# Performance work log

Measured on AMD Instinct MI355X. Metric: run time of the kernel, lower is better.

Reference implementation:

```python
import jax, jax.numpy as jnp
import numpy as np

B = 4096      # batch
F = 16        # num fields
V = 20000     # field vocab size
E = 64        # embed size
HID = 1024    # hidden width (all hidden layers equal, required by the reshape trick)
NODE_IN = F * E  # 1024
NL = 3        # number of hidden layers stacked into attention (len(layer_sizes)-2)


def _xavier(key, shape):
    fan_in, fan_out = shape[0], shape[1]
    lim = np.sqrt(6.0 / (fan_in + fan_out)).astype(np.float32)
    return jax.random.uniform(key, shape, jnp.float32, -lim, lim)


def setup_inputs() -> dict:
    key = jax.random.key(0)
    ks = jax.random.split(key, 8)
    idx = jax.random.randint(ks[0], (B, F), 0, V)
    emb = _xavier(ks[1], (V, E))  # share init shape, then tile per-field via fold_in
    emb = jnp.stack([_xavier(jax.random.fold_in(ks[1], f), (V, E)) for f in range(F)], axis=0)  # [F,V,E]
    w0 = _xavier(ks[2], (NODE_IN, HID)); b0 = jnp.zeros((HID,), jnp.float32)
    w1 = _xavier(ks[3], (HID, HID));     b1 = jnp.zeros((HID,), jnp.float32)
    w2 = _xavier(ks[4], (HID, HID));     b2 = jnp.zeros((HID,), jnp.float32)
    w3 = _xavier(ks[5], (HID, HID));     b3 = jnp.zeros((HID,), jnp.float32)
    w_final = _xavier(ks[6], (2 * HID, 1)); b_final = jnp.zeros((1,), jnp.float32)
    return {"idx": idx, "emb": emb, "w0": w0, "b0": b0, "w1": w1, "b1": b1,
            "w2": w2, "b2": b2, "w3": w3, "b3": b3,
            "w_final": w_final, "b_final": b_final}


def reference(idx, emb, w0, b0, w1, b1, w2, b2, w3, b3, w_final, b_final):
    bsz = idx.shape[0]
    # sparse one-hot @ embed == gather: [B,F,E] -> [B, F*E]
    xw = emb[jnp.arange(F)[None, :], idx].reshape(bsz, F * E)
    # MLP stack (dropout in test mode: keep_prob=1, i.e. identity)
    l0 = jax.nn.relu(xw @ w0 + b0)
    l1 = jax.nn.relu(l0 @ w1 + b1)
    l2 = jax.nn.relu(l1 @ w2 + b2)
    l_final = jax.nn.relu(l2 @ w3 + b3)
    # faithful reproduction of tf.concat(axis=0) then reshape([-1, NL, HID])
    cat = jnp.concatenate([l0, l1, l2], axis=0)          # [NL*B, HID]
    Hm = cat.reshape(bsz, NL, HID)                        # H[b,j] = cat[NL*b + j]
    mask = 1.0 - jnp.eye(NL, dtype=Hm.dtype)              # zero diagonal
    S = jnp.einsum('bih,bjh->bij', Hm, Hm) * mask         # [B, NL, NL]
    A = jax.nn.softmax(S, axis=-1)                        # attention over layers
    G = jnp.einsum('bij,bjh->bh', A, Hm)                  # reduce_sum(A@H, axis=1)
    M = jnp.concatenate([l_final, G], axis=1)             # [B, 2*HID]
    out = (M @ w_final + b_final).squeeze(-1)             # logits [B]
    return out
```

## Files before the change

kernel.cpp:

```cpp
#include <hip/hip_runtime.h>
#include <hip/hip_bf16.h>
#include <stdint.h>

#define B_SZ 4096
#define F_N 16
#define V_SZ 20000
#define E_SZ 64
#define HID 1024

typedef __attribute__((ext_vector_type(8))) _Float16 f16x8;
typedef __attribute__((ext_vector_type(4))) _Float16 f16x4;
typedef __attribute__((ext_vector_type(4))) float f32x4;

__device__ __forceinline__ void gload16(const void* g, void* l) {
  __builtin_amdgcn_global_load_lds(
      (const __attribute__((address_space(1))) void*)g,
      (__attribute__((address_space(3))) void*)l, 16, 0, 0);
}

__device__ __forceinline__ int s3(int r) { return (r ^ (r >> 3)) & 7; }

__global__ __launch_bounds__(256) void prep(
    const int* __restrict__ idx, const float* __restrict__ emb,
    const float* __restrict__ w0, const float* __restrict__ w1,
    const float* __restrict__ w2, const float* __restrict__ w3,
    _Float16* __restrict__ wt, _Float16* __restrict__ xw) {
  const int cb = blockIdx.x;
  const int t = threadIdx.x;
  if (cb < 2048) {
    const int z = cb >> 9, rem = cb & 511;
    const float* w = (z == 0) ? w0 : (z == 1) ? w1 : (z == 2) ? w2 : w3;
    _Float16* outp = wt + (size_t)z * HID * HID;
    __shared__ float tile[64][33];
    const int k0 = (rem >> 5) * 64, n0 = (rem & 31) * 32;
    const int c = t & 31;
#pragma unroll
    for (int q = 0; q < 8; ++q) {
      int r = (t >> 5) + q * 8;
      tile[r][c] = w[(size_t)(k0 + r) * HID + n0 + c];
    }
    __syncthreads();
#pragma unroll
    for (int q = 0; q < 4; ++q) {
      int s = t + q * 256;
      int n = s >> 5, c2 = s & 31;
      _Float16 lo = (_Float16)tile[2 * c2][n];
      _Float16 hi = (_Float16)tile[2 * c2 + 1][n];
      union { _Float16 h[2]; uint32_t u; } p;
      p.h[0] = lo; p.h[1] = hi;
      *(uint32_t*)(outp + (size_t)(n0 + n) * HID + k0 + 2 * c2) = p.u;
    }
  } else {
    int i = (cb - 2048) * 256 + t;
    int b = i >> 8;
    int r = i & 255;
    int f = r >> 4;
    int e4 = r & 15;
    int id = idx[b * F_N + f];
    float4 v = *(const float4*)(emb + ((size_t)f * V_SZ + id) * E_SZ + e4 * 4);
    f16x4 h = {(_Float16)v.x, (_Float16)v.y, (_Float16)v.z, (_Float16)v.w};
    *(f16x4*)(xw + (size_t)b * HID + r * 4) = h;
  }
}

__global__ __launch_bounds__(512) void gemm_mfma(
    const _Float16* __restrict__ A, const _Float16* __restrict__ Wt,
    const float* __restrict__ bias, _Float16* __restrict__ C) {
  __shared__ __align__(16) _Float16 sh[2][2][128 * 64];
#define AS(b) (sh[b][0])
#define BS(b) (sh[b][1])

  const int t = threadIdx.x;
  const int l = ((blockIdx.x & 7) << 5) | (blockIdx.x >> 3);
  const int bm = (l >> 3) * 128, bn = (l & 7) * 128;

  const int w = t >> 6, lane = t & 63;
  const int wk = w & 1, wn = (w >> 1) & 1, wm = w >> 2;
  const int lr = lane & 15, lg = lane >> 4;

  const int srow = t >> 3, cdst = t & 7;
  const int csrc = cdst ^ s3(srow);
  const _Float16* ga0 = A + (size_t)(bm + srow) * HID + csrc * 8;
  const _Float16* gb0 = Wt + (size_t)(bn + srow) * HID + csrc * 8;
  const int ld0 = t * 8, ld1 = t * 8 + 4096;

  int aoff[4], boff[4];
#pragma unroll
  for (int i = 0; i < 4; i++) {
    int ra = wm * 64 + i * 16 + lr;
    aoff[i] = ra * 64 + (((wk * 4 + lg) ^ s3(ra)) * 8);
    int rb = wn * 64 + i * 16 + lr;
    boff[i] = rb * 64 + (((wk * 4 + lg) ^ s3(rb)) * 8);
  }

  f32x4 acc[4][4] = {};

#define STAGE(buf, ko)                                   \
  gload16(ga0 + (ko), &AS(buf)[ld0]);                    \
  gload16(ga0 + (ko) + (size_t)64 * HID, &AS(buf)[ld1]); \
  gload16(gb0 + (ko), &BS(buf)[ld0]);                    \
  gload16(gb0 + (ko) + (size_t)64 * HID, &BS(buf)[ld1]);

  STAGE(0, 0)

  for (int tI = 0; tI < 16; ++tI) {
    const int cur = tI & 1;
    if (tI < 15) {
      STAGE(cur ^ 1, (tI + 1) * 64)
    }
    if (tI < 15)
      asm volatile("s_waitcnt vmcnt(4)" ::: "memory");
    else
      asm volatile("s_waitcnt vmcnt(0)" ::: "memory");
    asm volatile("s_barrier" ::: "memory");

    f16x8 a[4], b[4];
#pragma unroll
    for (int mi = 0; mi < 4; mi++) a[mi] = *(const f16x8*)&AS(cur)[aoff[mi]];
#pragma unroll
    for (int ni = 0; ni < 4; ni++) b[ni] = *(const f16x8*)&BS(cur)[boff[ni]];
#pragma unroll
    for (int mi = 0; mi < 4; mi++)
#pragma unroll
      for (int ni = 0; ni < 4; ni++)
        acc[mi][ni] = __builtin_amdgcn_mfma_f32_16x16x32_f16(
            a[mi], b[ni], acc[mi][ni], 0, 0, 0);

    asm volatile("s_barrier" ::: "memory");
  }
#undef STAGE

  float* red = (float*)&sh[0][0][0];
  float* R = red + ((wm << 1) | wn) * 4096;
  if (wk == 1) {
#pragma unroll
    for (int mi = 0; mi < 4; mi++)
#pragma unroll
      for (int ni = 0; ni < 4; ni++) {
        int col = ni * 16 + lr;
        int rb = mi * 4 + lg;
        *(f32x4*)&R[col * 64 + ((rb ^ (col & 15)) << 2)] = acc[mi][ni];
      }
  }
  asm volatile("s_barrier" ::: "memory");
  if (wk == 0) {
#pragma unroll
    for (int mi = 0; mi < 4; mi++)
#pragma unroll
      for (int ni = 0; ni < 4; ni++) {
        int col = ni * 16 + lr;
        int rb = mi * 4 + lg;
        f32x4 p = *(const f32x4*)&R[col * 64 + ((rb ^ (col & 15)) << 2)];
        acc[mi][ni] += p;
      }
#pragma unroll
    for (int ni = 0; ni < 4; ni++) {
      int col = bn + wn * 64 + ni * 16 + lr;
      float bv = bias[col];
#pragma unroll
      for (int mi = 0; mi < 4; mi++) {
        int rbase = bm + wm * 64 + mi * 16 + lg * 4;
#pragma unroll
        for (int j = 0; j < 4; j++) {
          float x = acc[mi][ni][j] + bv;
          x = x > 0.f ? x : 0.f;
          C[(size_t)(rbase + j) * HID + col] = (_Float16)x;
        }
      }
    }
  }
#undef AS
#undef BS
}

__global__ __launch_bounds__(256) void attn_final(
    const _Float16* __restrict__ cat, const _Float16* __restrict__ lf,
    const float* __restrict__ wf, const float* __restrict__ bfin,
    float* __restrict__ out) {
  const int wave = threadIdx.x >> 6;
  const int lane = threadIdx.x & 63;
  const int b = blockIdx.x * 4 + wave;

  const _Float16* h0 = cat + (size_t)(3 * b + 0) * 1024;
  const _Float16* h1 = cat + (size_t)(3 * b + 1) * 1024;
  const _Float16* h2 = cat + (size_t)(3 * b + 2) * 1024;
  const _Float16* lfr = lf + (size_t)b * 1024;

  float s01 = 0.f, s02 = 0.f, s12 = 0.f;
  float d0 = 0.f, d1 = 0.f, d2 = 0.f, dl = 0.f;

#pragma unroll
  for (int q = 0; q < 2; ++q) {
    int e8 = (lane + q * 64) * 8;
    f16x8 a0 = *(const f16x8*)(h0 + e8);
    f16x8 a1 = *(const f16x8*)(h1 + e8);
    f16x8 a2 = *(const f16x8*)(h2 + e8);
    f16x8 al = *(const f16x8*)(lfr + e8);
    float4 u0a = *(const float4*)(wf + e8);
    float4 u0b = *(const float4*)(wf + e8 + 4);
    float4 u1a = *(const float4*)(wf + 1024 + e8);
    float4 u1b = *(const float4*)(wf + 1024 + e8 + 4);
    float wf0[8] = {u0a.x, u0a.y, u0a.z, u0a.w, u0b.x, u0b.y, u0b.z, u0b.w};
    float wf1[8] = {u1a.x, u1a.y, u1a.z, u1a.w, u1b.x, u1b.y, u1b.z, u1b.w};
#pragma unroll
    for (int j = 0; j < 8; ++j) {
      float p0 = (float)a0[j], p1 = (float)a1[j], p2 = (float)a2[j];
      float pl = (float)al[j];
      s01 = fmaf(p0, p1, s01);
      s02 = fmaf(p0, p2, s02);
      s12 = fmaf(p1, p2, s12);
      d0 = fmaf(p0, wf1[j], d0);
      d1 = fmaf(p1, wf1[j], d1);
      d2 = fmaf(p2, wf1[j], d2);
      dl = fmaf(pl, wf0[j], dl);
    }
  }

#pragma unroll
  for (int m = 1; m < 64; m <<= 1) {
    s01 += __shfl_xor(s01, m);
    s02 += __shfl_xor(s02, m);
    s12 += __shfl_xor(s12, m);
    d0 += __shfl_xor(d0, m);
    d1 += __shfl_xor(d1, m);
    d2 += __shfl_xor(d2, m);
    dl += __shfl_xor(dl, m);
  }

  if (lane == 0) {
    float c0 = 0.f, c1 = 0.f, c2 = 0.f;
    {
      float m = fmaxf(0.f, fmaxf(s01, s02));
      float e0 = expf(0.f - m), e1 = expf(s01 - m), e2 = expf(s02 - m);
      float inv = 1.f / (e0 + e1 + e2);
      c0 += e0 * inv; c1 += e1 * inv; c2 += e2 * inv;
    }
    {
      float m = fmaxf(s01, fmaxf(0.f, s12));
      float e0 = expf(s01 - m), e1 = expf(0.f - m), e2 = expf(s12 - m);
      float inv = 1.f / (e0 + e1 + e2);
      c0 += e0 * inv; c1 += e1 * inv; c2 += e2 * inv;
    }
    {
      float m = fmaxf(s02, fmaxf(s12, 0.f));
      float e0 = expf(s02 - m), e1 = expf(s12 - m), e2 = expf(0.f - m);
      float inv = 1.f / (e0 + e1 + e2);
      c0 += e0 * inv; c1 += e1 * inv; c2 += e2 * inv;
    }
    out[b] = dl + c0 * d0 + c1 * d1 + c2 * d2 + bfin[0];
  }
}

extern "C" void kernel_launch(void* const* d_in, const int* in_sizes, int n_in,
                              void* d_out, int out_size, void* d_ws,
                              size_t ws_size, hipStream_t stream) {
  const int* idx = (const int*)d_in[0];
  const float* emb = (const float*)d_in[1];
  const float* w0 = (const float*)d_in[2];
  const float* b0 = (const float*)d_in[3];
  const float* w1 = (const float*)d_in[4];
  const float* b1 = (const float*)d_in[5];
  const float* w2 = (const float*)d_in[6];
  const float* b2 = (const float*)d_in[7];
  const float* w3 = (const float*)d_in[8];
  const float* b3 = (const float*)d_in[9];
  const float* wf = (const float*)d_in[10];
  const float* bfin = (const float*)d_in[11];
  float* out = (float*)d_out;

  const size_t RB = (size_t)B_SZ * HID;
  const size_t WSZ = (size_t)HID * HID;

  _Float16* wt = (_Float16*)d_ws;
  _Float16* xw16 = wt + 4 * WSZ;
  _Float16* cat16 = xw16 + RB;
  _Float16* lf16 = cat16 + 3 * RB;

  prep<<<6144, 256, 0, stream>>>(idx, emb, w0, w1, w2, w3, wt, xw16);

  gemm_mfma<<<256, 512, 0, stream>>>(xw16, wt + 0 * WSZ, b0, cat16);
  gemm_mfma<<<256, 512, 0, stream>>>(cat16, wt + 1 * WSZ, b1, cat16 + RB);
  gemm_mfma<<<256, 512, 0, stream>>>(cat16 + RB, wt + 2 * WSZ, b2,
                                     cat16 + 2 * RB);
  gemm_mfma<<<256, 512, 0, stream>>>(cat16 + 2 * RB, wt + 3 * WSZ, b3, lf16);

  attn_final<<<B_SZ / 4, 256, 0, stream>>>(cat16, lf16, wf, bfin, out);
}
```

Measured before the change: 73.23 us.

## Overlap weight conversion with previous GEMM and load B directly to registers

Converting and transposing the next layer's weights now happens in extra blocks (256..511) of the preceding GEMM launch, so the prep kernel only handles w0 and the embedding gather. The GEMM now reads B fragments straight from global memory into registers instead of staging them through LDS. A becomes a triple-buffered LDS pipeline with explicit waitcnt, sched barriers and setprio around the MFMAs. This is meant to hide prep cost and cut LDS traffic and barriers, at the cost of uncoalesced global B loads and heavier register use.

```diff
diff --git a/kernel.cpp b/kernel.cpp
--- a/kernel.cpp
+++ b/kernel.cpp
@@ -22,36 +22,31 @@
 
 __global__ __launch_bounds__(256) void prep(
     const int* __restrict__ idx, const float* __restrict__ emb,
-    const float* __restrict__ w0, const float* __restrict__ w1,
-    const float* __restrict__ w2, const float* __restrict__ w3,
-    _Float16* __restrict__ wt, _Float16* __restrict__ xw) {
+    const float* __restrict__ w0, _Float16* __restrict__ wt0,
+    _Float16* __restrict__ xw) {
   const int cb = blockIdx.x;
   const int t = threadIdx.x;
-  if (cb < 2048) {
-    const int z = cb >> 9, rem = cb & 511;
-    const float* w = (z == 0) ? w0 : (z == 1) ? w1 : (z == 2) ? w2 : w3;
-    _Float16* outp = wt + (size_t)z * HID * HID;
+  if (cb < 512) {
     __shared__ float tile[64][33];
-    const int k0 = (rem >> 5) * 64, n0 = (rem & 31) * 32;
+    const int k0 = (cb >> 5) * 64, n0 = (cb & 31) * 32;
     const int c = t & 31;
 #pragma unroll
     for (int q = 0; q < 8; ++q) {
       int r = (t >> 5) + q * 8;
-      tile[r][c] = w[(size_t)(k0 + r) * HID + n0 + c];
+      tile[r][c] = w0[(size_t)(k0 + r) * HID + n0 + c];
     }
     __syncthreads();
 #pragma unroll
     for (int q = 0; q < 4; ++q) {
       int s = t + q * 256;
       int n = s >> 5, c2 = s & 31;
-      _Float16 lo = (_Float16)tile[2 * c2][n];
-      _Float16 hi = (_Float16)tile[2 * c2 + 1][n];
       union { _Float16 h[2]; uint32_t u; } p;
-      p.h[0] = lo; p.h[1] = hi;
-      *(uint32_t*)(outp + (size_t)(n0 + n) * HID + k0 + 2 * c2) = p.u;
+      p.h[0] = (_Float16)tile[2 * c2][n];
+      p.h[1] = (_Float16)tile[2 * c2 + 1][n];
+      *(uint32_t*)(wt0 + (size_t)(n0 + n) * HID + k0 + 2 * c2) = p.u;
     }
   } else {
-    int i = (cb - 2048) * 256 + t;
+    int i = (cb - 512) * 256 + t;
     int b = i >> 8;
     int r = i & 255;
     int f = r >> 4;
@@ -65,12 +60,34 @@
 
 __global__ __launch_bounds__(512) void gemm_mfma(
     const _Float16* __restrict__ A, const _Float16* __restrict__ Wt,
-    const float* __restrict__ bias, _Float16* __restrict__ C) {
-  __shared__ __align__(16) _Float16 sh[2][2][128 * 64];
-#define AS(b) (sh[b][0])
-#define BS(b) (sh[b][1])
-
+    const float* __restrict__ bias, _Float16* __restrict__ C,
+    const float* __restrict__ wnx, _Float16* __restrict__ wtnx) {
+  __shared__ __align__(16) char shraw[65536];
   const int t = threadIdx.x;
+
+  if (blockIdx.x >= 256) {
+    const int cv = blockIdx.x - 256;
+    float (*tile)[65] = (float(*)[65])shraw;
+    const int k0 = (cv >> 4) * 64, n0 = (cv & 15) * 64;
+    const int c = t & 63;
+#pragma unroll
+    for (int q = 0; q < 8; ++q) {
+      int r = (t >> 6) + q * 8;
+      tile[r][c] = wnx[(size_t)(k0 + r) * HID + n0 + c];
+    }
+    __syncthreads();
+    {
+      int n = t >> 3, ch = t & 7;
+      f16x8 v;
+#pragma unroll
+      for (int j = 0; j < 8; ++j) v[j] = (_Float16)tile[ch * 8 + j][n];
+      *(f16x8*)(wtnx + (size_t)(n0 + n) * HID + k0 + ch * 8) = v;
+    }
+    return;
+  }
+
+#define AS(b) ((_Float16*)(shraw + (b) * 16384))
+
   const int l = ((blockIdx.x & 7) << 5) | (blockIdx.x >> 3);
   const int bm = (l >> 3) * 128, bn = (l & 7) * 128;
 
@@ -81,56 +98,83 @@
   const int srow = t >> 3, cdst = t & 7;
   const int csrc = cdst ^ s3(srow);
   const _Float16* ga0 = A + (size_t)(bm + srow) * HID + csrc * 8;
-  const _Float16* gb0 = Wt + (size_t)(bn + srow) * HID + csrc * 8;
   const int ld0 = t * 8, ld1 = t * 8 + 4096;
 
-  int aoff[4], boff[4];
+  int aoff[4];
 #pragma unroll
   for (int i = 0; i < 4; i++) {
     int ra = wm * 64 + i * 16 + lr;
     aoff[i] = ra * 64 + (((wk * 4 + lg) ^ s3(ra)) * 8);
-    int rb = wn * 64 + i * 16 + lr;
-    boff[i] = rb * 64 + (((wk * 4 + lg) ^ s3(rb)) * 8);
-  }
+  }
+
+  const _Float16* gB[4];
+#pragma unroll
+  for (int ni = 0; ni < 4; ni++)
+    gB[ni] = Wt + (size_t)(bn + wn * 64 + ni * 16 + lr) * HID + wk * 32 + lg * 8;
 
   f32x4 acc[4][4] = {};
+  f16x8 bE[4], bO[4];
 
 #define STAGE(buf, ko)                                   \
   gload16(ga0 + (ko), &AS(buf)[ld0]);                    \
-  gload16(ga0 + (ko) + (size_t)64 * HID, &AS(buf)[ld1]); \
-  gload16(gb0 + (ko), &BS(buf)[ld0]);                    \
-  gload16(gb0 + (ko) + (size_t)64 * HID, &BS(buf)[ld1]);
+  gload16(ga0 + (ko) + (size_t)64 * HID, &AS(buf)[ld1]);
+
+#define LOADB(dst, ko)                                             \
+  _Pragma("unroll") for (int ni = 0; ni < 4; ni++)                 \
+      dst[ni] = *(const f16x8*)(gB[ni] + (ko));
+
+#define COMPUTE(BUF, BREG)                                                   \
+  {                                                                          \
+    f16x8 a[4];                                                              \
+    _Pragma("unroll") for (int mi = 0; mi < 4; mi++)                         \
+        a[mi] = *(const f16x8*)&AS(BUF)[aoff[mi]];                           \
+    __builtin_amdgcn_s_setprio(1);                                           \
+    _Pragma("unroll") for (int mi = 0; mi < 4; mi++)                         \
+        _Pragma("unroll") for (int ni = 0; ni < 4; ni++)                     \
+            acc[mi][ni] = __builtin_amdgcn_mfma_f32_16x16x32_f16(            \
+                a[mi], BREG[ni], acc[mi][ni], 0, 0, 0);                      \
+    __builtin_amdgcn_s_setprio(0);                                           \
+  }
 
   STAGE(0, 0)
-
-  for (int tI = 0; tI < 16; ++tI) {
-    const int cur = tI & 1;
-    if (tI < 15) {
-      STAGE(cur ^ 1, (tI + 1) * 64)
-    }
-    if (tI < 15)
-      asm volatile("s_waitcnt vmcnt(4)" ::: "memory");
+  __builtin_amdgcn_sched_barrier(0);
+  LOADB(bE, 0)
+  __builtin_amdgcn_sched_barrier(0);
+  STAGE(1, 64)
+
+#pragma unroll
+  for (int u = 0; u < 8; ++u) {
+    const int ta = 2 * u, tb = 2 * u + 1;
+    asm volatile("s_waitcnt vmcnt(2)" ::: "memory");
+    asm volatile("s_barrier" ::: "memory");
+    LOADB(bO, (ta + 1) * 64)
+    __builtin_amdgcn_sched_barrier(0);
+    if (ta + 2 < 16) {
+      STAGE((ta + 2) % 3, (ta + 2) * 64)
+    }
+    __builtin_amdgcn_sched_barrier(0);
+    COMPUTE(ta % 3, bE)
+    if (tb == 15)
+      asm volatile("s_waitcnt vmcnt(0)" ::: "memory");
     else
-      asm volatile("s_waitcnt vmcnt(0)" ::: "memory");
+      asm volatile("s_waitcnt vmcnt(2)" ::: "memory");
     asm volatile("s_barrier" ::: "memory");
-
-    f16x8 a[4], b[4];
-#pragma unroll
-    for (int mi = 0; mi < 4; mi++) a[mi] = *(const f16x8*)&AS(cur)[aoff[mi]];
-#pragma unroll
-    for (int ni = 0; ni < 4; ni++) b[ni] = *(const f16x8*)&BS(cur)[boff[ni]];
-#pragma unroll
-    for (int mi = 0; mi < 4; mi++)
-#pragma unroll
-      for (int ni = 0; ni < 4; ni++)
-        acc[mi][ni] = __builtin_amdgcn_mfma_f32_16x16x32_f16(
-            a[mi], b[ni], acc[mi][ni], 0, 0, 0);
-
-    asm volatile("s_barrier" ::: "memory");
-  }
+    if (tb + 1 < 16) {
+      LOADB(bE, (tb + 1) * 64)
+    }
+    __builtin_amdgcn_sched_barrier(0);
+    if (tb + 2 < 16) {
+      STAGE((tb + 2) % 3, (tb + 2) * 64)
+    }
+    __builtin_amdgcn_sched_barrier(0);
+    COMPUTE(tb % 3, bO)
+  }
+#undef COMPUTE
+#undef LOADB
 #undef STAGE
 
-  float* red = (float*)&sh[0][0][0];
+  asm volatile("s_barrier" ::: "memory");
+  float* red = (float*)shraw;
   float* R = red + ((wm << 1) | wn) * 4096;
   if (wk == 1) {
 #pragma unroll
@@ -170,7 +214,6 @@
     }
   }
 #undef AS
-#undef BS
 }
 
 __global__ __launch_bounds__(256) void attn_final(
@@ -276,13 +319,17 @@
   _Float16* cat16 = xw16 + RB;
   _Float16* lf16 = cat16 + 3 * RB;
 
-  prep<<<6144, 256, 0, stream>>>(idx, emb, w0, w1, w2, w3, wt, xw16);
-
-  gemm_mfma<<<256, 512, 0, stream>>>(xw16, wt + 0 * WSZ, b0, cat16);
-  gemm_mfma<<<256, 512, 0, stream>>>(cat16, wt + 1 * WSZ, b1, cat16 + RB);
-  gemm_mfma<<<256, 512, 0, stream>>>(cat16 + RB, wt + 2 * WSZ, b2,
-                                     cat16 + 2 * RB);
-  gemm_mfma<<<256, 512, 0, stream>>>(cat16 + 2 * RB, wt + 3 * WSZ, b3, lf16);
+  prep<<<4608, 256, 0, stream>>>(idx, emb, w0, wt, xw16);
+
+  gemm_mfma<<<512, 512, 0, stream>>>(xw16, wt + 0 * WSZ, b0, cat16,
+                                     w1, wt + 1 * WSZ);
+  gemm_mfma<<<512, 512, 0, stream>>>(cat16, wt + 1 * WSZ, b1, cat16 + RB,
+                                     w2, wt + 2 * WSZ);
+  gemm_mfma<<<512, 512, 0, stream>>>(cat16 + RB, wt + 2 * WSZ, b2,
+                                     cat16 + 2 * RB, w3, wt + 3 * WSZ);
+  gemm_mfma<<<256, 512, 0, stream>>>(cat16 + 2 * RB, wt + 3 * WSZ, b3, lf16,
+                                     (const float*)nullptr,
+                                     (_Float16*)nullptr);
 
   attn_final<<<B_SZ / 4, 256, 0, stream>>>(cat16, lf16, wf, bfin, out);
 }
```

After: 124.3 us. 1.7x slower.

## Deepen GEMM K-loop to four LDS stages with register double-buffered fragments

Applied to the files above, without the earlier changes.

The MFMA GEMM main loop moves from a double-buffered LDS ring to a four-slot ring with two tiles in flight, and is unrolled by two. Register fragments are now double-buffered, so the LDS reads for the next tile are issued before the MFMAs for the current tile, with s_setprio raised around the MFMA block. This aims to hide global-load and LDS latency and to drop the second barrier per iteration. In exchange it uses 128KB of LDS per block and more registers, which could limit occupancy.

```diff
diff --git a/kernel.cpp b/kernel.cpp
--- a/kernel.cpp
+++ b/kernel.cpp
@@ -44,10 +44,9 @@
     for (int q = 0; q < 4; ++q) {
       int s = t + q * 256;
       int n = s >> 5, c2 = s & 31;
-      _Float16 lo = (_Float16)tile[2 * c2][n];
-      _Float16 hi = (_Float16)tile[2 * c2 + 1][n];
       union { _Float16 h[2]; uint32_t u; } p;
-      p.h[0] = lo; p.h[1] = hi;
+      p.h[0] = (_Float16)tile[2 * c2][n];
+      p.h[1] = (_Float16)tile[2 * c2 + 1][n];
       *(uint32_t*)(outp + (size_t)(n0 + n) * HID + k0 + 2 * c2) = p.u;
     }
   } else {
@@ -66,9 +65,9 @@
 __global__ __launch_bounds__(512) void gemm_mfma(
     const _Float16* __restrict__ A, const _Float16* __restrict__ Wt,
     const float* __restrict__ bias, _Float16* __restrict__ C) {
-  __shared__ __align__(16) _Float16 sh[2][2][128 * 64];
-#define AS(b) (sh[b][0])
-#define BS(b) (sh[b][1])
+  __shared__ __align__(16) char shraw[131072];
+#define AS(b) ((_Float16*)(shraw + (b) * 32768))
+#define BS(b) ((_Float16*)(shraw + (b) * 32768 + 16384))
 
   const int t = threadIdx.x;
   const int l = ((blockIdx.x & 7) << 5) | (blockIdx.x >> 3);
@@ -94,6 +93,7 @@
   }
 
   f32x4 acc[4][4] = {};
+  f16x8 aE[4], bE[4], aO[4], bO[4];
 
 #define STAGE(buf, ko)                                   \
   gload16(ga0 + (ko), &AS(buf)[ld0]);                    \
@@ -101,36 +101,60 @@
   gload16(gb0 + (ko), &BS(buf)[ld0]);                    \
   gload16(gb0 + (ko) + (size_t)64 * HID, &BS(buf)[ld1]);
 
+#define LOADFRAG(AF, BF, buf)                                      \
+  _Pragma("unroll") for (int i = 0; i < 4; i++) {                  \
+    AF[i] = *(const f16x8*)&AS(buf)[aoff[i]];                      \
+    BF[i] = *(const f16x8*)&BS(buf)[boff[i]];                      \
+  }
+
+#define COMPUTE(AF, BF)                                                      \
+  {                                                                          \
+    __builtin_amdgcn_s_setprio(1);                                          \
+    _Pragma("unroll") for (int mi = 0; mi < 4; mi++)                         \
+        _Pragma("unroll") for (int ni = 0; ni < 4; ni++)                     \
+            acc[mi][ni] = __builtin_amdgcn_mfma_f32_16x16x32_f16(            \
+                AF[mi], BF[ni], acc[mi][ni], 0, 0, 0);                       \
+    __builtin_amdgcn_s_setprio(0);                                          \
+  }
+
   STAGE(0, 0)
-
-  for (int tI = 0; tI < 16; ++tI) {
-    const int cur = tI & 1;
-    if (tI < 15) {
-      STAGE(cur ^ 1, (tI + 1) * 64)
-    }
-    if (tI < 15)
+  STAGE(1, 64)
+  asm volatile("s_waitcnt vmcnt(4)" ::: "memory");
+  asm volatile("s_barrier" ::: "memory");
+  LOADFRAG(aE, bE, 0)
+
+#pragma unroll
+  for (int u = 0; u < 8; ++u) {
+    const int ta = 2 * u, tb = 2 * u + 1;
+    if (ta + 2 < 16) {
+      STAGE((ta + 2) & 3, (ta + 2) * 64)
+    }
+    if (ta < 14)
       asm volatile("s_waitcnt vmcnt(4)" ::: "memory");
-    else
+    else if (ta == 14)
       asm volatile("s_waitcnt vmcnt(0)" ::: "memory");
     asm volatile("s_barrier" ::: "memory");
-
-    f16x8 a[4], b[4];
-#pragma unroll
-    for (int mi = 0; mi < 4; mi++) a[mi] = *(const f16x8*)&AS(cur)[aoff[mi]];
-#pragma unroll
-    for (int ni = 0; ni < 4; ni++) b[ni] = *(const f16x8*)&BS(cur)[boff[ni]];
-#pragma unroll
-    for (int mi = 0; mi < 4; mi++)
-#pragma unroll
-      for (int ni = 0; ni < 4; ni++)
-        acc[mi][ni] = __builtin_amdgcn_mfma_f32_16x16x32_f16(
-            a[mi], b[ni], acc[mi][ni], 0, 0, 0);
-
+    LOADFRAG(aO, bO, (ta + 1) & 3)
+    COMPUTE(aE, bE)
+    if (tb + 2 < 16) {
+      STAGE((tb + 2) & 3, (tb + 2) * 64)
+    }
+    if (tb < 14)
+      asm volatile("s_waitcnt vmcnt(4)" ::: "memory");
+    else if (tb == 14)
+      asm volatile("s_waitcnt vmcnt(0)" ::: "memory");
     asm volatile("s_barrier" ::: "memory");
-  }
+    if (tb < 15) {
+      LOADFRAG(aE, bE, (tb + 1) & 3)
+    }
+    COMPUTE(aO, bO)
+  }
+#undef COMPUTE
+#undef LOADFRAG
 #undef STAGE
 
-  float* red = (float*)&sh[0][0][0];
+  asm volatile("s_barrier" ::: "memory");
+  float* red = (float*)shraw;
   float* R = red + ((wm << 1) | wn) * 4096;
   if (wk == 1) {
 #pragma unroll
```

Result: no change. 74.11 us (+1.2%).

## Overlap next-layer weight transpose with GEMM and vectorize epilogue stores

Applied to the files above, without the earlier changes.

The prep kernel now converts and transposes only w0. Each GEMM launch gets 256 extra blocks that transpose and convert the next layer's weights into fp16, so that work shares the launch with the current GEMM instead of running serially beforehand. The MFMA operand order is swapped so each lane holds four consecutive columns, which allows a float4 bias load and 8-byte f16x4 output stores instead of scalar 2-byte stores. The extra blocks compete with GEMM blocks for CUs and shared memory, and the reduction layout is changed to match the transposed accumulator.

```diff
diff --git a/kernel.cpp b/kernel.cpp
--- a/kernel.cpp
+++ b/kernel.cpp
@@ -22,36 +22,31 @@
 
 __global__ __launch_bounds__(256) void prep(
     const int* __restrict__ idx, const float* __restrict__ emb,
-    const float* __restrict__ w0, const float* __restrict__ w1,
-    const float* __restrict__ w2, const float* __restrict__ w3,
-    _Float16* __restrict__ wt, _Float16* __restrict__ xw) {
+    const float* __restrict__ w0, _Float16* __restrict__ wt0,
+    _Float16* __restrict__ xw) {
   const int cb = blockIdx.x;
   const int t = threadIdx.x;
-  if (cb < 2048) {
-    const int z = cb >> 9, rem = cb & 511;
-    const float* w = (z == 0) ? w0 : (z == 1) ? w1 : (z == 2) ? w2 : w3;
-    _Float16* outp = wt + (size_t)z * HID * HID;
+  if (cb < 512) {
     __shared__ float tile[64][33];
-    const int k0 = (rem >> 5) * 64, n0 = (rem & 31) * 32;
+    const int k0 = (cb >> 5) * 64, n0 = (cb & 31) * 32;
     const int c = t & 31;
 #pragma unroll
     for (int q = 0; q < 8; ++q) {
       int r = (t >> 5) + q * 8;
-      tile[r][c] = w[(size_t)(k0 + r) * HID + n0 + c];
+      tile[r][c] = w0[(size_t)(k0 + r) * HID + n0 + c];
     }
     __syncthreads();
 #pragma unroll
     for (int q = 0; q < 4; ++q) {
       int s = t + q * 256;
       int n = s >> 5, c2 = s & 31;
-      _Float16 lo = (_Float16)tile[2 * c2][n];
-      _Float16 hi = (_Float16)tile[2 * c2 + 1][n];
       union { _Float16 h[2]; uint32_t u; } p;
-      p.h[0] = lo; p.h[1] = hi;
-      *(uint32_t*)(outp + (size_t)(n0 + n) * HID + k0 + 2 * c2) = p.u;
+      p.h[0] = (_Float16)tile[2 * c2][n];
+      p.h[1] = (_Float16)tile[2 * c2 + 1][n];
+      *(uint32_t*)(wt0 + (size_t)(n0 + n) * HID + k0 + 2 * c2) = p.u;
     }
   } else {
-    int i = (cb - 2048) * 256 + t;
+    int i = (cb - 512) * 256 + t;
     int b = i >> 8;
     int r = i & 255;
     int f = r >> 4;
@@ -65,12 +60,35 @@
 
 __global__ __launch_bounds__(512) void gemm_mfma(
     const _Float16* __restrict__ A, const _Float16* __restrict__ Wt,
-    const float* __restrict__ bias, _Float16* __restrict__ C) {
-  __shared__ __align__(16) _Float16 sh[2][2][128 * 64];
-#define AS(b) (sh[b][0])
-#define BS(b) (sh[b][1])
-
+    const float* __restrict__ bias, _Float16* __restrict__ C,
+    const float* __restrict__ wnx, _Float16* __restrict__ wtnx) {
+  __shared__ __align__(16) char shraw[65536];
   const int t = threadIdx.x;
+
+  if (blockIdx.x >= 256) {
+    const int cv = blockIdx.x - 256;
+    float (*tile)[65] = (float(*)[65])shraw;
+    const int k0 = (cv >> 4) * 64, n0 = (cv & 15) * 64;
+    const int c = t & 63;
+#pragma unroll
+    for (int q = 0; q < 8; ++q) {
+      int r = (t >> 6) + q * 8;
+      tile[r][c] = wnx[(size_t)(k0 + r) * HID + n0 + c];
+    }
+    __syncthreads();
+    {
+      int n = t >> 3, ch = t & 7;
+      f16x8 v;
+#pragma unroll
+      for (int j = 0; j < 8; ++j) v[j] = (_Float16)tile[ch * 8 + j][n];
+      *(f16x8*)(wtnx + (size_t)(n0 + n) * HID + k0 + ch * 8) = v;
+    }
+    return;
+  }
+
+#define AS(b) ((_Float16*)(shraw + (b) * 32768))
+#define BS(b) ((_Float16*)(shraw + (b) * 32768 + 16384))
+
   const int l = ((blockIdx.x & 7) << 5) | (blockIdx.x >> 3);
   const int bm = (l >> 3) * 128, bn = (l & 7) * 128;
 
@@ -124,22 +142,22 @@
 #pragma unroll
       for (int ni = 0; ni < 4; ni++)
         acc[mi][ni] = __builtin_amdgcn_mfma_f32_16x16x32_f16(
-            a[mi], b[ni], acc[mi][ni], 0, 0, 0);
+            b[ni], a[mi], acc[mi][ni], 0, 0, 0);
 
     asm volatile("s_barrier" ::: "memory");
   }
 #undef STAGE
 
-  float* red = (float*)&sh[0][0][0];
+  float* red = (float*)shraw;
   float* R = red + ((wm << 1) | wn) * 4096;
   if (wk == 1) {
 #pragma unroll
     for (int mi = 0; mi < 4; mi++)
 #pragma unroll
       for (int ni = 0; ni < 4; ni++) {
-        int col = ni * 16 + lr;
-        int rb = mi * 4 + lg;
-        *(f32x4*)&R[col * 64 + ((rb ^ (col & 15)) << 2)] = acc[mi][ni];
+        int u = mi * 16 + lr;
+        int vb = ni * 4 + lg;
+        *(f32x4*)&R[u * 64 + ((vb ^ lr) << 2)] = acc[mi][ni];
       }
   }
   asm volatile("s_barrier" ::: "memory");
@@ -148,24 +166,28 @@
     for (int mi = 0; mi < 4; mi++)
 #pragma unroll
       for (int ni = 0; ni < 4; ni++) {
-        int col = ni * 16 + lr;
-        int rb = mi * 4 + lg;
-        f32x4 p = *(const f32x4*)&R[col * 64 + ((rb ^ (col & 15)) << 2)];
+        int u = mi * 16 + lr;
+        int vb = ni * 4 + lg;
+        f32x4 p = *(const f32x4*)&R[u * 64 + ((vb ^ lr) << 2)];
         acc[mi][ni] += p;
       }
 #pragma unroll
     for (int ni = 0; ni < 4; ni++) {
-      int col = bn + wn * 64 + ni * 16 + lr;
-      float bv = bias[col];
+      int colb = bn + wn * 64 + ni * 16 + lg * 4;
+      float4 bv = *(const float4*)&bias[colb];
 #pragma unroll
       for (int mi = 0; mi < 4; mi++) {
-        int rbase = bm + wm * 64 + mi * 16 + lg * 4;
-#pragma unroll
-        for (int j = 0; j < 4; j++) {
-          float x = acc[mi][ni][j] + bv;
-          x = x > 0.f ? x : 0.f;
-          C[(size_t)(rbase + j) * HID + col] = (_Float16)x;
-        }
+        int row = bm + wm * 64 + mi * 16 + lr;
+        f16x4 hv;
+        float x0 = acc[mi][ni][0] + bv.x;
+        float x1 = acc[mi][ni][1] + bv.y;
+        float x2 = acc[mi][ni][2] + bv.z;
+        float x3 = acc[mi][ni][3] + bv.w;
+        hv[0] = (_Float16)(x0 > 0.f ? x0 : 0.f);
+        hv[1] = (_Float16)(x1 > 0.f ? x1 : 0.f);
+        hv[2] = (_Float16)(x2 > 0.f ? x2 : 0.f);
+        hv[3] = (_Float16)(x3 > 0.f ? x3 : 0.f);
+        *(f16x4*)&C[(size_t)row * HID + colb] = hv;
       }
     }
   }
@@ -276,13 +298,17 @@
   _Float16* cat16 = xw16 + RB;
   _Float16* lf16 = cat16 + 3 * RB;
 
-  prep<<<6144, 256, 0, stream>>>(idx, emb, w0, w1, w2, w3, wt, xw16);
-
-  gemm_mfma<<<256, 512, 0, stream>>>(xw16, wt + 0 * WSZ, b0, cat16);
-  gemm_mfma<<<256, 512, 0, stream>>>(cat16, wt + 1 * WSZ, b1, cat16 + RB);
-  gemm_mfma<<<256, 512, 0, stream>>>(cat16 + RB, wt + 2 * WSZ, b2,
-                                     cat16 + 2 * RB);
-  gemm_mfma<<<256, 512, 0, stream>>>(cat16 + 2 * RB, wt + 3 * WSZ, b3, lf16);
+  prep<<<4608, 256, 0, stream>>>(idx, emb, w0, wt, xw16);
+
+  gemm_mfma<<<512, 512, 0, stream>>>(xw16, wt + 0 * WSZ, b0, cat16,
+                                     w1, wt + 1 * WSZ);
+  gemm_mfma<<<512, 512, 0, stream>>>(cat16, wt + 1 * WSZ, b1, cat16 + RB,
+                                     w2, wt + 2 * WSZ);
+  gemm_mfma<<<512, 512, 0, stream>>>(cat16 + RB, wt + 2 * WSZ, b2,
+                                     cat16 + 2 * RB, w3, wt + 3 * WSZ);
+  gemm_mfma<<<256, 512, 0, stream>>>(cat16 + 2 * RB, wt + 3 * WSZ, b3, lf16,
+                                     (const float*)nullptr,
+                                     (_Float16*)nullptr);
 
   attn_final<<<B_SZ / 4, 256, 0, stream>>>(cat16, lf16, wf, bfin, out);
 }
```

Result: slower. 76.73 us (+4.8%).
